# Kernel optimization log

Measured on AMD Instinct MI355X. Metric: run time of the kernel, lower is better.

## Reference

```python
import jax, jax.numpy as jnp
import numpy as np

B, C_IN, T, N_VERTEX = 2, 64, 12, 2048
KS, C_OUT = 3, 64
NNZ = 98304  # Ks * n_vertex * avg_degree(16)


def setup_inputs() -> dict:
    key = jax.random.key(0)
    k0, k1, k2, k3, k4, k5 = jax.random.split(key, 6)
    x = jax.random.normal(k0, (B, C_IN, T, N_VERTEX), jnp.float32)
    # kaiming-uniform-ish init for weight [Ks, c_in, c_out]
    bound_w = float(np.sqrt(6.0 / C_IN))
    weight = jax.random.uniform(k1, (KS, C_IN, C_OUT), jnp.float32, -bound_w, bound_w)
    bound_b = float(1.0 / np.sqrt(C_OUT))
    bias = jax.random.uniform(k2, (C_OUT,), jnp.float32, -bound_b, bound_b)
    # sparse chebconv_filter in COO: shape [n_vertex, Ks*n_vertex]
    filter_rows = jax.random.randint(k3, (NNZ,), 0, N_VERTEX)
    filter_cols = jax.random.randint(k4, (NNZ,), 0, KS * N_VERTEX)
    filter_vals = jax.random.normal(k5, (NNZ,), jnp.float32) * 0.1
    return dict(x=x, weight=weight, bias=bias, filter_vals=filter_vals,
                filter_rows=filter_rows, filter_cols=filter_cols)


def reference(x, weight, bias, filter_vals, filter_rows, filter_cols):
    b, c_in, t, n = x.shape
    ks, _, c_out = weight.shape
    # dense GEMM: [B*T*n (row-major flatten of B,c_in,T,n keeping last dim c_in), c_in] @ [c_in, Ks*c_out]
    xw = x.reshape(-1, c_in) @ weight.reshape(c_in, ks * c_out)  # [B*c_in*T*n/c_in, Ks*c_out]
    xw = xw.reshape(n * ks, -1)                                  # [n*Ks, B*T*c_out]
    # spmm with COO filter [n, n*Ks]: gather columns, scale, scatter-add to rows
    gathered = filter_vals[:, None] * xw[filter_cols]            # [nnz, B*T*c_out]
    y = jax.ops.segment_sum(gathered, filter_rows, num_segments=N_VERTEX)  # [n, B*T*c_out]
    return y.reshape(-1, c_out) + bias                           # [n*B*T, c_out]
```

## Files before the change

kernel.cpp:

```cpp
#include <hip/hip_runtime.h>
#include <hip/hip_bf16.h>

#define NV      2048
#define NNZ_    98304
#define GROWS   49152
#define KDIM    64
#define WCOLS   192
#define MCOLS   1536
#define BUCKET  128

typedef __attribute__((ext_vector_type(8))) short  short8;
typedef __attribute__((ext_vector_type(8))) unsigned short ushort8;
typedef __attribute__((ext_vector_type(4))) float  float4v;

__device__ __forceinline__ float b2f(unsigned short h) {
    return __uint_as_float(((unsigned int)h) << 16);
}
__device__ __forceinline__ unsigned short f2b(float f) {
    return __bfloat16_as_ushort(__float2bfloat16(f));
}

__global__ __launch_bounds__(256) void scatter_kernel(
    const int4* __restrict__ rows4, const int4* __restrict__ cols4,
    const float4* __restrict__ vals4, const float* __restrict__ wf,
    int* __restrict__ cnt, int2* __restrict__ sedge,
    unsigned short* __restrict__ wt)
{
    if (blockIdx.x == NNZ_ / 1024) {
        for (int i = 0; i < 48; i++) {
            const int e = threadIdx.x + 256 * i;
            const int k = e / WCOLS, n = e - k * WCOLS;
            wt[n * KDIM + k] = f2b(wf[e]);
        }
        return;
    }
    const int t = blockIdx.x * 256 + threadIdx.x;
    const int4   r = rows4[t];
    const int4   c = cols4[t];
    const float4 v = vals4[t];
    int p;
    p = atomicAdd(&cnt[r.x], 1); if (p < BUCKET) sedge[r.x * BUCKET + p] = make_int2(c.x * MCOLS, __float_as_int(v.x));
    p = atomicAdd(&cnt[r.y], 1); if (p < BUCKET) sedge[r.y * BUCKET + p] = make_int2(c.y * MCOLS, __float_as_int(v.y));
    p = atomicAdd(&cnt[r.z], 1); if (p < BUCKET) sedge[r.z * BUCKET + p] = make_int2(c.z * MCOLS, __float_as_int(v.z));
    p = atomicAdd(&cnt[r.w], 1); if (p < BUCKET) sedge[r.w * BUCKET + p] = make_int2(c.w * MCOLS, __float_as_int(v.w));
}

__global__ __launch_bounds__(256) void gemm_kernel(
    const float* __restrict__ xf, const unsigned short* __restrict__ wt,
    unsigned short* __restrict__ y1)
{
    __shared__ unsigned short Wt[WCOLS * 72];
    __shared__ unsigned short Xs[64 * 72];
    const int tid = threadIdx.x;
    const int r0  = blockIdx.x * 64;

#pragma unroll
    for (int u = 0; u < 2; u++) {
        const int ch = tid + 256 * u;
        const float4 x0 = *(const float4*)(xf + (size_t)r0 * KDIM + ch * 8);
        const float4 x1 = *(const float4*)(xf + (size_t)r0 * KDIM + ch * 8 + 4);
        ushort8 p;
        p[0]=f2b(x0.x); p[1]=f2b(x0.y); p[2]=f2b(x0.z); p[3]=f2b(x0.w);
        p[4]=f2b(x1.x); p[5]=f2b(x1.y); p[6]=f2b(x1.z); p[7]=f2b(x1.w);
        const int row = ch >> 3, col = (ch & 7) * 8;
        *(ushort8*)&Xs[row * 72 + col] = p;
    }
#pragma unroll
    for (int u = 0; u < 6; u++) {
        const int ch = tid + 256 * u;
        const ushort8 p = *(const ushort8*)(wt + ch * 8);
        const int row = ch >> 3, col = (ch & 7) * 8;
        *(ushort8*)&Wt[row * 72 + col] = p;
    }
    __syncthreads();

    const int lane = tid & 63;
    const int mt   = tid >> 6;
    const int q    = lane >> 4;
    const int c    = lane & 15;

    const short8 a0 = *(const short8*)&Xs[(mt * 16 + c) * 72 + q * 8];
    const short8 a1 = *(const short8*)&Xs[(mt * 16 + c) * 72 + 32 + q * 8];

    float4v acc[12];
#pragma unroll
    for (int nt = 0; nt < 12; nt++) {
        const short8 b0 = *(const short8*)&Wt[(nt * 16 + c) * 72 + q * 8];
        const short8 b1 = *(const short8*)&Wt[(nt * 16 + c) * 72 + 32 + q * 8];
        float4v d = {0.f, 0.f, 0.f, 0.f};
        d = __builtin_amdgcn_mfma_f32_16x16x32_bf16(a0, b0, d, 0, 0, 0);
        d = __builtin_amdgcn_mfma_f32_16x16x32_bf16(a1, b1, d, 0, 0, 0);
        acc[nt] = d;
    }

    const int rbase = r0 + mt * 16 + q * 4;
#pragma unroll
    for (int nt = 0; nt < 12; nt++) {
        const int col = nt * 16 + c;
#pragma unroll
        for (int r = 0; r < 4; r++)
            y1[(size_t)(rbase + r) * WCOLS + col] = f2b(acc[nt][r]);
    }
}

__global__ __launch_bounds__(64) void spmm_kernel(
    const unsigned short* __restrict__ Y,
    const int* __restrict__ cnt,
    const int2* __restrict__ sedge,
    const float* __restrict__ bias,
    float* __restrict__ out)
{
    const int b    = blockIdx.x;
    const int slab = b & 7;
    const int row  = b >> 3;
    const int lane = threadIdx.x;
    if (lane >= 48) return;

    int n = cnt[row];
    if (n > BUCKET) n = BUCKET;
    const int2* se = sedge + row * BUCKET;
    const int base = slab * WCOLS + 4 * lane;

    float a0 = 0.f, a1 = 0.f, a2 = 0.f, a3 = 0.f;
    int i = 0;
    for (; i + 4 <= n; i += 4) {
        const int2 e0 = se[i], e1 = se[i + 1], e2 = se[i + 2], e3 = se[i + 3];
        const ushort4 p0 = *(const ushort4*)(Y + e0.x + base);
        const ushort4 p1 = *(const ushort4*)(Y + e1.x + base);
        const ushort4 p2 = *(const ushort4*)(Y + e2.x + base);
        const ushort4 p3 = *(const ushort4*)(Y + e3.x + base);
        const float v0 = __int_as_float(e0.y), v1 = __int_as_float(e1.y);
        const float v2 = __int_as_float(e2.y), v3 = __int_as_float(e3.y);
        a0 += v0 * b2f(p0.x) + v1 * b2f(p1.x) + v2 * b2f(p2.x) + v3 * b2f(p3.x);
        a1 += v0 * b2f(p0.y) + v1 * b2f(p1.y) + v2 * b2f(p2.y) + v3 * b2f(p3.y);
        a2 += v0 * b2f(p0.z) + v1 * b2f(p1.z) + v2 * b2f(p2.z) + v3 * b2f(p3.z);
        a3 += v0 * b2f(p0.w) + v1 * b2f(p1.w) + v2 * b2f(p2.w) + v3 * b2f(p3.w);
    }
    for (; i < n; i++) {
        const int2 e = se[i];
        const ushort4 p = *(const ushort4*)(Y + e.x + base);
        const float v = __int_as_float(e.y);
        a0 += v * b2f(p.x); a1 += v * b2f(p.y);
        a2 += v * b2f(p.z); a3 += v * b2f(p.w);
    }

    const float4 bb = *(const float4*)(bias + ((4 * lane) & 63));
    float4 o;
    o.x = a0 + bb.x; o.y = a1 + bb.y; o.z = a2 + bb.z; o.w = a3 + bb.w;
    *(float4*)(out + (size_t)row * MCOLS + base) = o;
}

extern "C" void kernel_launch(void* const* d_in, const int* in_sizes, int n_in,
                              void* d_out, int out_size, void* d_ws, size_t ws_size,
                              hipStream_t stream) {
    const float* x    = (const float*)d_in[0];
    const float* wgt  = (const float*)d_in[1];
    const float* bias = (const float*)d_in[2];
    const float* fval = (const float*)d_in[3];
    const int* frow   = (const int*)d_in[4];
    const int* fcol   = (const int*)d_in[5];

    int* cnt = (int*)d_ws;
    int2* sedge = (int2*)(cnt + 2048);
    unsigned short* wt = (unsigned short*)(sedge + NV * BUCKET);
    unsigned short* y1 = wt + 12288;

    hipMemsetAsync(cnt, 0, 2048 * sizeof(int), stream);
    scatter_kernel<<<NNZ_ / 1024 + 1, 256, 0, stream>>>(
        (const int4*)frow, (const int4*)fcol, (const float4*)fval, wgt,
        cnt, sedge, wt);
    gemm_kernel  <<<GROWS / 64, 256, 0, stream>>>(x, wt, y1);
    spmm_kernel  <<<NV * 8,     64,  0, stream>>>(y1, cnt, sedge, bias, (float*)d_out);
}
```

Baseline: 127.7 us.

## Reorder SpMM before GEMM to shrink gathered data and intermediate

Uses associativity to apply the sparse filter directly to the input x (gathering 512-float rows) first, then multiply the reduced result by the weight with MFMA, fusing bias into the GEMM epilogue. The old order materialized a 3x wider bf16 intermediate (Ks*c_out columns) that the SpMM gathered from. The new order gathers fp32 x rows, which cuts gather traffic and shrinks the GEMM to a third of the rows. The intermediate is still rounded to bf16, and the SpMM now uses scalar per-lane loads.

```diff
diff --git a/kernel.cpp b/kernel.cpp
--- a/kernel.cpp
+++ b/kernel.cpp
@@ -3,10 +3,9 @@
 
 #define NV      2048
 #define NNZ_    98304
-#define GROWS   49152
 #define KDIM    64
 #define WCOLS   192
-#define MCOLS   1536
+#define ZROWS   16384
 #define BUCKET  128
 
 typedef __attribute__((ext_vector_type(8))) short  short8;
@@ -39,31 +38,61 @@
     const int4   c = cols4[t];
     const float4 v = vals4[t];
     int p;
-    p = atomicAdd(&cnt[r.x], 1); if (p < BUCKET) sedge[r.x * BUCKET + p] = make_int2(c.x * MCOLS, __float_as_int(v.x));
-    p = atomicAdd(&cnt[r.y], 1); if (p < BUCKET) sedge[r.y * BUCKET + p] = make_int2(c.y * MCOLS, __float_as_int(v.y));
-    p = atomicAdd(&cnt[r.z], 1); if (p < BUCKET) sedge[r.z * BUCKET + p] = make_int2(c.z * MCOLS, __float_as_int(v.z));
-    p = atomicAdd(&cnt[r.w], 1); if (p < BUCKET) sedge[r.w * BUCKET + p] = make_int2(c.w * MCOLS, __float_as_int(v.w));
+    p = atomicAdd(&cnt[r.x], 1); if (p < BUCKET) sedge[r.x * BUCKET + p] = make_int2(c.x * 512, __float_as_int(v.x));
+    p = atomicAdd(&cnt[r.y], 1); if (p < BUCKET) sedge[r.y * BUCKET + p] = make_int2(c.y * 512, __float_as_int(v.y));
+    p = atomicAdd(&cnt[r.z], 1); if (p < BUCKET) sedge[r.z * BUCKET + p] = make_int2(c.z * 512, __float_as_int(v.z));
+    p = atomicAdd(&cnt[r.w], 1); if (p < BUCKET) sedge[r.w * BUCKET + p] = make_int2(c.w * 512, __float_as_int(v.w));
 }
 
-__global__ __launch_bounds__(256) void gemm_kernel(
-    const float* __restrict__ xf, const unsigned short* __restrict__ wt,
-    unsigned short* __restrict__ y1)
+__global__ __launch_bounds__(64) void spmmx_kernel(
+    const float* __restrict__ xf,
+    const int* __restrict__ cnt,
+    const int2* __restrict__ sedge,
+    unsigned short* __restrict__ zb)
+{
+    const int b    = blockIdx.x;
+    const int g    = b & 7;
+    const int row  = b >> 3;
+    const int lane = threadIdx.x;
+
+    int n = cnt[row];
+    if (n > BUCKET) n = BUCKET;
+    const int2* se = sedge + row * BUCKET;
+    const int off = g * KDIM + lane;
+
+    float acc = 0.f;
+    int i = 0;
+    for (; i + 4 <= n; i += 4) {
+        const int2 e0 = se[i], e1 = se[i + 1], e2 = se[i + 2], e3 = se[i + 3];
+        const float x0 = xf[e0.x + off];
+        const float x1 = xf[e1.x + off];
+        const float x2 = xf[e2.x + off];
+        const float x3 = xf[e3.x + off];
+        acc += __int_as_float(e0.y) * x0 + __int_as_float(e1.y) * x1
+             + __int_as_float(e2.y) * x2 + __int_as_float(e3.y) * x3;
+    }
+    for (; i < n; i++) {
+        const int2 e = se[i];
+        acc += __int_as_float(e.y) * xf[e.x + off];
+    }
+    zb[(size_t)(row * 8 + g) * KDIM + lane] = f2b(acc);
+}
+
+__global__ __launch_bounds__(256) void gemm2_kernel(
+    const unsigned short* __restrict__ zb, const unsigned short* __restrict__ wt,
+    const float* __restrict__ bias, float* __restrict__ out)
 {
     __shared__ unsigned short Wt[WCOLS * 72];
-    __shared__ unsigned short Xs[64 * 72];
+    __shared__ unsigned short Zs[64 * 72];
     const int tid = threadIdx.x;
-    const int r0  = blockIdx.x * 64;
+    const int m0  = blockIdx.x * 64;
 
 #pragma unroll
     for (int u = 0; u < 2; u++) {
         const int ch = tid + 256 * u;
-        const float4 x0 = *(const float4*)(xf + (size_t)r0 * KDIM + ch * 8);
-        const float4 x1 = *(const float4*)(xf + (size_t)r0 * KDIM + ch * 8 + 4);
-        ushort8 p;
-        p[0]=f2b(x0.x); p[1]=f2b(x0.y); p[2]=f2b(x0.z); p[3]=f2b(x0.w);
-        p[4]=f2b(x1.x); p[5]=f2b(x1.y); p[6]=f2b(x1.z); p[7]=f2b(x1.w);
+        const ushort8 p = *(const ushort8*)(zb + (size_t)m0 * KDIM + ch * 8);
         const int row = ch >> 3, col = (ch & 7) * 8;
-        *(ushort8*)&Xs[row * 72 + col] = p;
+        *(ushort8*)&Zs[row * 72 + col] = p;
     }
 #pragma unroll
     for (int u = 0; u < 6; u++) {
@@ -79,8 +108,8 @@
     const int q    = lane >> 4;
     const int c    = lane & 15;
 
-    const short8 a0 = *(const short8*)&Xs[(mt * 16 + c) * 72 + q * 8];
-    const short8 a1 = *(const short8*)&Xs[(mt * 16 + c) * 72 + 32 + q * 8];
+    const short8 a0 = *(const short8*)&Zs[(mt * 16 + c) * 72 + q * 8];
+    const short8 a1 = *(const short8*)&Zs[(mt * 16 + c) * 72 + 32 + q * 8];
 
     float4v acc[12];
 #pragma unroll
@@ -93,61 +122,15 @@
         acc[nt] = d;
     }
 
-    const int rbase = r0 + mt * 16 + q * 4;
+    const int rbase = m0 + mt * 16 + q * 4;
 #pragma unroll
     for (int nt = 0; nt < 12; nt++) {
         const int col = nt * 16 + c;
+        const float bb = bias[col & 63];
 #pragma unroll
         for (int r = 0; r < 4; r++)
-            y1[(size_t)(rbase + r) * WCOLS + col] = f2b(acc[nt][r]);
+            out[(size_t)(rbase + r) * WCOLS + col] = acc[nt][r] + bb;
     }
-}
-
-__global__ __launch_bounds__(64) void spmm_kernel(
-    const unsigned short* __restrict__ Y,
-    const int* __restrict__ cnt,
-    const int2* __restrict__ sedge,
-    const float* __restrict__ bias,
-    float* __restrict__ out)
-{
-    const int b    = blockIdx.x;
-    const int slab = b & 7;
-    const int row  = b >> 3;
-    const int lane = threadIdx.x;
-    if (lane >= 48) return;
-
-    int n = cnt[row];
-    if (n > BUCKET) n = BUCKET;
-    const int2* se = sedge + row * BUCKET;
-    const int base = slab * WCOLS + 4 * lane;
-
-    float a0 = 0.f, a1 = 0.f, a2 = 0.f, a3 = 0.f;
-    int i = 0;
-    for (; i + 4 <= n; i += 4) {
-        const int2 e0 = se[i], e1 = se[i + 1], e2 = se[i + 2], e3 = se[i + 3];
-        const ushort4 p0 = *(const ushort4*)(Y + e0.x + base);
-        const ushort4 p1 = *(const ushort4*)(Y + e1.x + base);
-        const ushort4 p2 = *(const ushort4*)(Y + e2.x + base);
-        const ushort4 p3 = *(const ushort4*)(Y + e3.x + base);
-        const float v0 = __int_as_float(e0.y), v1 = __int_as_float(e1.y);
-        const float v2 = __int_as_float(e2.y), v3 = __int_as_float(e3.y);
-        a0 += v0 * b2f(p0.x) + v1 * b2f(p1.x) + v2 * b2f(p2.x) + v3 * b2f(p3.x);
-        a1 += v0 * b2f(p0.y) + v1 * b2f(p1.y) + v2 * b2f(p2.y) + v3 * b2f(p3.y);
-        a2 += v0 * b2f(p0.z) + v1 * b2f(p1.z) + v2 * b2f(p2.z) + v3 * b2f(p3.z);
-        a3 += v0 * b2f(p0.w) + v1 * b2f(p1.w) + v2 * b2f(p2.w) + v3 * b2f(p3.w);
-    }
-    for (; i < n; i++) {
-        const int2 e = se[i];
-        const ushort4 p = *(const ushort4*)(Y + e.x + base);
-        const float v = __int_as_float(e.y);
-        a0 += v * b2f(p.x); a1 += v * b2f(p.y);
-        a2 += v * b2f(p.z); a3 += v * b2f(p.w);
-    }
-
-    const float4 bb = *(const float4*)(bias + ((4 * lane) & 63));
-    float4 o;
-    o.x = a0 + bb.x; o.y = a1 + bb.y; o.z = a2 + bb.z; o.w = a3 + bb.w;
-    *(float4*)(out + (size_t)row * MCOLS + base) = o;
 }
 
 extern "C" void kernel_launch(void* const* d_in, const int* in_sizes, int n_in,
@@ -163,12 +146,12 @@
     int* cnt = (int*)d_ws;
     int2* sedge = (int2*)(cnt + 2048);
     unsigned short* wt = (unsigned short*)(sedge + NV * BUCKET);
-    unsigned short* y1 = wt + 12288;
+    unsigned short* zb = wt + 12288;
 
     hipMemsetAsync(cnt, 0, 2048 * sizeof(int), stream);
     scatter_kernel<<<NNZ_ / 1024 + 1, 256, 0, stream>>>(
         (const int4*)frow, (const int4*)fcol, (const float4*)fval, wgt,
         cnt, sedge, wt);
-    gemm_kernel  <<<GROWS / 64, 256, 0, stream>>>(x, wt, y1);
-    spmm_kernel  <<<NV * 8,     64,  0, stream>>>(y1, cnt, sedge, bias, (float*)d_out);
+    spmmx_kernel <<<NV * 8,    64,  0, stream>>>(x, cnt, sedge, zb);
+    gemm2_kernel <<<ZROWS / 64, 256, 0, stream>>>(zb, wt, bias, (float*)d_out);
 }
```

New measurement: 109.6 us. 14.2% less time.
